# Kernel tuning notes

Hardware: AMD Instinct MI355X
Metric: run time of the kernel (lower is better)

## Reference

```python
import jax, jax.numpy as jnp
from jax import lax
import numpy as np

T, B, HIDDEN, MLPW, DATA = 256, 4096, 64, 128, 8
TSCALE = 1.0

def lipswish(x):
    return 0.909 * jax.nn.silu(x)

def setup_inputs() -> dict:
    key = jax.random.key(0)
    ks = jax.random.split(key, 8)
    def lin(k, i, o):
        return jax.random.normal(k, (i, o), jnp.float32) / np.float32(np.sqrt(i))
    inp = dict(
        ts=jnp.linspace(0.0, 1.0, T, dtype=jnp.float32),
        batch_size=B,
        dW=jax.random.normal(ks[0], (T - 1, B, HIDDEN), jnp.float32),
        drift_W0=lin(ks[1], 1 + HIDDEN, MLPW), drift_b0=jnp.zeros((MLPW,), jnp.float32),
        drift_W1=lin(ks[2], MLPW, MLPW),       drift_b1=jnp.zeros((MLPW,), jnp.float32),
        drift_Wo=lin(ks[3], MLPW, HIDDEN),     drift_bo=jnp.zeros((HIDDEN,), jnp.float32),
        diff_W0=lin(ks[4], 1 + HIDDEN, MLPW),  diff_b0=jnp.zeros((MLPW,), jnp.float32),
        diff_W1=lin(ks[5], MLPW, MLPW),        diff_b1=jnp.zeros((MLPW,), jnp.float32),
        diff_Wo=lin(ks[6], MLPW, HIDDEN),      diff_bo=jnp.zeros((HIDDEN,), jnp.float32),
        readout_W=lin(ks[7], HIDDEN, DATA),    readout_b=jnp.zeros((DATA,), jnp.float32),
    )
    return inp

def reference(ts, batch_size, dW,
              drift_W0, drift_b0, drift_W1, drift_b1, drift_Wo, drift_bo,
              diff_W0, diff_b0, diff_W1, diff_b1, diff_Wo, diff_bo,
              readout_W, readout_b):
    dt = ts[1] - ts[0]  # uniform grid, dt_scale = 1.0

    def mlp(tx, W0, b0, W1, b1, Wo, bo):
        h = lipswish(tx @ W0 + b0)
        h = lipswish(h @ W1 + b1)
        return TSCALE * jnp.tanh(h @ Wo + bo)  # tanh-clamped output

    def f_and_g(t, x):
        tcol = t * jnp.ones((x.shape[0], 1), x.dtype)
        tx = jnp.concatenate([tcol, x], axis=1)  # (B, 1+H)
        f = mlp(tx, drift_W0, drift_b0, drift_W1, drift_b1, drift_Wo, drift_bo)
        g = mlp(tx, diff_W0, diff_b0, diff_W1, diff_b1, diff_Wo, diff_bo)  # diagonal noise
        return f, g

    x0 = jnp.ones((batch_size, HIDDEN), jnp.float32)  # fixed initial point
    f0, g0 = f_and_g(ts[0], x0)
    dWs = dW * jnp.sqrt(dt)  # Brownian increments N(0, dt)

    # Reversible Heun (Stratonovich):
    #   zhat_{n+1} = 2 z_n - zhat_n + f(t_n, zhat_n) dt + g(t_n, zhat_n) dW_n
    #   z_{n+1}    = z_n + 0.5 (f_n + f_{n+1}) dt + 0.5 (g_n + g_{n+1}) dW_n
    def step(carry, inp):
        z, zhat, f, g = carry
        t_next, dw = inp
        zhat_n = 2.0 * z - zhat + f * dt + g * dw
        f_n, g_n = f_and_g(t_next, zhat_n)
        z_n = z + 0.5 * (f + f_n) * dt + 0.5 * (g + g_n) * dw
        return (z_n, zhat_n, f_n, g_n), z_n

    _, zs = lax.scan(step, (x0, x0, f0, g0), (ts[1:], dWs))
    xs = jnp.concatenate([x0[None], zs], axis=0)  # (T, B, H)
    ys = jnp.einsum('tbh,hd->tbd', xs, readout_W) + readout_b  # (T, B, D)
    ys = ys.transpose(1, 0, 2)  # (B, T, D)
    ts_e = jnp.broadcast_to(ts[None, :, None], (batch_size, ts.shape[0], 1))
    # linear_interpolation_coeffs on NaN-free data returns the values unchanged
    return jnp.concatenate([ts_e, ys], axis=2)  # (B, T, 1+D)
```

## Files before the change

### kernel.cpp

```cpp
#include <hip/hip_runtime.h>
#include <math.h>

#define T_STEPS 256
#define BATCH   4096
#define HID     64
#define MW      128
#define DOUT    8
#define RPB     16
#define NTH     512
#define AS      72
#define HS      136

typedef _Float16 half8 __attribute__((ext_vector_type(8)));
typedef float    f32x4 __attribute__((ext_vector_type(4)));

__device__ __forceinline__ float fast_rcp(float x) { return __builtin_amdgcn_rcpf(x); }
__device__ __forceinline__ float lipswish(float x) {
    float e = __expf(-x);
    return 0.909f * x * fast_rcp(1.0f + e);
}
__device__ __forceinline__ float fast_tanh(float x) {
    float e = __expf(2.0f * x);
    return 1.0f - 2.0f * fast_rcp(e + 1.0f);
}

#define MFMA(a, b, c) __builtin_amdgcn_mfma_f32_16x16x32_f16((a), (b), (c), 0, 0, 0)


__global__ __launch_bounds__(NTH, 1)
void sde_kernel(const float* __restrict__ ts,
                const float* __restrict__ dW,
                const float* __restrict__ dW0, const float* __restrict__ db0,
                const float* __restrict__ dW1, const float* __restrict__ db1,
                const float* __restrict__ dWo, const float* __restrict__ dbo,
                const float* __restrict__ gW0, const float* __restrict__ gb0,
                const float* __restrict__ gW1, const float* __restrict__ gb1,
                const float* __restrict__ gWo, const float* __restrict__ gbo,
                const float* __restrict__ rW,  const float* __restrict__ rb,
                float* __restrict__ out)
{
    __shared__ _Float16 Ain_hi[RPB][AS];
    __shared__ _Float16 Ain_lo[RPB][AS];
    __shared__ _Float16 h1b[2][RPB][HS];
    __shared__ _Float16 h2b[2][RPB][HS];
    __shared__ _Float16 zb[2][RPB][AS];
    __shared__ float    bias1t[2 * MW];
    __shared__ float    tsS[T_STEPS];

    const int tid  = threadIdx.x;
    const int lane = tid & 63;
    const int wid  = tid >> 6;
    const int l15  = lane & 15;
    const int quad = lane >> 4;
    const int mlp  = wid >> 2;
    const int nq   = wid & 3;
    const int rowbase = blockIdx.x * RPB;

    for (int i = tid; i < T_STEPS; i += NTH) tsS[i] = ts[i];

    const float t0   = ts[0];
    const float dt   = ts[1] - t0;
    const float sqdt = sqrtf(dt);

    const float* W0 = mlp ? gW0 : dW0;
    const float* W1 = mlp ? gW1 : dW1;

    half8 bw1[2][2], bw2[4][2];
    #pragma unroll
    for (int kt = 0; kt < 2; ++kt)
        #pragma unroll
        for (int nt = 0; nt < 2; ++nt) {
            half8 v;
            #pragma unroll
            for (int j = 0; j < 8; ++j) {
                const int k = kt * 32 + quad * 8 + j;
                const int n = nq * 32 + nt * 16 + l15;
                v[j] = (_Float16)W0[(1 + k) * MW + n];
            }
            bw1[kt][nt] = v;
        }
    #pragma unroll
    for (int kt = 0; kt < 4; ++kt)
        #pragma unroll
        for (int nt = 0; nt < 2; ++nt) {
            half8 v;
            #pragma unroll
            for (int j = 0; j < 8; ++j) {
                const int k = kt * 32 + quad * 8 + j;
                const int n = nq * 32 + nt * 16 + l15;
                v[j] = (_Float16)W1[k * MW + n];
            }
            bw2[kt][nt] = v;
        }

    float b2v[2];
    {
        const float* b1p = mlp ? gb1 : db1;
        #pragma unroll
        for (int nt = 0; nt < 2; ++nt) b2v[nt] = b1p[nq * 32 + nt * 16 + l15];
    }

    const int ucol = nq * 16 + l15;
    const int urow = quad * 4;

    half8 bw3f[4], bw3g[4];
    float b3f = 0.0f, b3g = 0.0f;
    float z[4], zh[4], fold[4], gold[4], dwr[4], dn[4];
    if (wid < 4) {
        #pragma unroll
        for (int kt = 0; kt < 4; ++kt) {
            half8 vf, vg;
            #pragma unroll
            for (int j = 0; j < 8; ++j) {
                const int k = kt * 32 + quad * 8 + j;
                vf[j] = (_Float16)dWo[k * HID + ucol];
                vg[j] = (_Float16)gWo[k * HID + ucol];
            }
            bw3f[kt] = vf;
            bw3g[kt] = vg;
        }
        b3f = dbo[ucol];
        b3g = gbo[ucol];
        #pragma unroll
        for (int i = 0; i < 4; ++i) {
            z[i] = 1.0f; zh[i] = 1.0f; dwr[i] = 0.0f;
            dn[i] = dW[(size_t)(rowbase + urow + i) * HID + ucol];
            Ain_hi[urow + i][ucol] = (_Float16)1.0f;
            Ain_lo[urow + i][ucol] = (_Float16)0.0f;
        }
    }

    half8 brd[2];
    float rbv = 0.0f;
    int   ocol = 0;
    if (wid == 4) {
        #pragma unroll
        for (int kt = 0; kt < 2; ++kt) {
            half8 v;
            #pragma unroll
            for (int j = 0; j < 8; ++j) {
                const int k = kt * 32 + quad * 8 + j;
                v[j] = (l15 < 8) ? (_Float16)rW[k * DOUT + l15] : (_Float16)0.0f;
            }
            brd[kt] = v;
        }
        rbv  = (l15 < 8) ? rb[l15] : 0.0f;
        ocol = (l15 == 8) ? 0 : (l15 + 1);
    }

    float b0s = 0.0f, w0s = 0.0f;
    if (tid >= 256) {
        const int idx = tid - 256;
        b0s = (idx < MW ? db0 : gb0)[idx & (MW - 1)];
        w0s = (idx < MW ? dW0 : gW0)[idx & (MW - 1)];
        bias1t[idx] = b0s + t0 * w0s;
    }
    __syncthreads();

    for (int n = 1; n <= T_STEPS; ++n) {
        {
            const int koff = quad * 8;
            half8 ah[2], al[2];
            #pragma unroll
            for (int kt = 0; kt < 2; ++kt) {
                ah[kt] = *(const half8*)&Ain_hi[l15][kt * 32 + koff];
                al[kt] = *(const half8*)&Ain_lo[l15][kt * 32 + koff];
            }
            f32x4 acc[2];
            #pragma unroll
            for (int nt = 0; nt < 2; ++nt) {
                const float b = bias1t[mlp * MW + nq * 32 + nt * 16 + l15];
                acc[nt] = (f32x4){b, b, b, b};
            }
            #pragma unroll
            for (int nt = 0; nt < 2; ++nt)
                #pragma unroll
                for (int kt = 0; kt < 2; ++kt) {
                    acc[nt] = MFMA(ah[kt], bw1[kt][nt], acc[nt]);
                    acc[nt] = MFMA(al[kt], bw1[kt][nt], acc[nt]);
                }
            #pragma unroll
            for (int nt = 0; nt < 2; ++nt)
                #pragma unroll
                for (int i2 = 0; i2 < 4; ++i2) {
                    const float v = lipswish(acc[nt][i2]);
                    h1b[mlp][quad * 4 + i2][nq * 32 + nt * 16 + l15] = (_Float16)v;
                }
        }
        __syncthreads();

        {
            half8 a[4];
            #pragma unroll
            for (int kt = 0; kt < 4; ++kt)
                a[kt] = *(const half8*)&h1b[mlp][l15][kt * 32 + quad * 8];
            f32x4 acc[2];
            #pragma unroll
            for (int nt = 0; nt < 2; ++nt)
                acc[nt] = (f32x4){b2v[nt], b2v[nt], b2v[nt], b2v[nt]};
            #pragma unroll
            for (int nt = 0; nt < 2; ++nt)
                #pragma unroll
                for (int kt = 0; kt < 4; ++kt)
                    acc[nt] = MFMA(a[kt], bw2[kt][nt], acc[nt]);
            #pragma unroll
            for (int nt = 0; nt < 2; ++nt)
                #pragma unroll
                for (int i2 = 0; i2 < 4; ++i2) {
                    const float v = lipswish(acc[nt][i2]);
                    h2b[mlp][quad * 4 + i2][nq * 32 + nt * 16 + l15] = (_Float16)v;
                }
        }
        __syncthreads();

        if (wid < 4) {
            half8 a[4];
            #pragma unroll
            for (int kt = 0; kt < 4; ++kt)
                a[kt] = *(const half8*)&h2b[0][l15][kt * 32 + quad * 8];
            f32x4 accF = (f32x4){b3f, b3f, b3f, b3f};
            #pragma unroll
            for (int kt = 0; kt < 4; ++kt)
                accF = MFMA(a[kt], bw3f[kt], accF);
            #pragma unroll
            for (int kt = 0; kt < 4; ++kt)
                a[kt] = *(const half8*)&h2b[1][l15][kt * 32 + quad * 8];
            f32x4 accG = (f32x4){b3g, b3g, b3g, b3g};
            #pragma unroll
            for (int kt = 0; kt < 4; ++kt)
                accG = MFMA(a[kt], bw3g[kt], accG);

            const int p = n & 1;
            const int np = (n < T_STEPS - 2) ? n : (T_STEPS - 2);
            #pragma unroll
            for (int i = 0; i < 4; ++i) {
                const float fn = fast_tanh(accF[i]);
                const float gn = fast_tanh(accG[i]);
                if (n > 1)
                    z[i] += 0.5f * (fold[i] + fn) * dt + 0.5f * (gold[i] + gn) * dwr[i];
                zb[p][urow + i][ucol] = (_Float16)z[i];
                if (n < T_STEPS) {
                    dwr[i] = dn[i] * sqdt;
                    dn[i]  = dW[(size_t)np * (BATCH * HID)
                                + (size_t)(rowbase + urow + i) * HID + ucol];
                    zh[i]  = 2.0f * z[i] - zh[i] + fn * dt + gn * dwr[i];
                    const _Float16 hi = (_Float16)zh[i];
                    Ain_hi[urow + i][ucol] = hi;
                    Ain_lo[urow + i][ucol] = (_Float16)(zh[i] - (float)hi);
                }
                fold[i] = fn; gold[i] = gn;
            }
        } else {
            if (wid == 4 && n >= 2) {
                const int koff = quad * 8, q = (n - 1) & 1, s = n - 2;
                half8 a0 = *(const half8*)&zb[q][l15][koff];
                half8 a1 = *(const half8*)&zb[q][l15][32 + koff];
                f32x4 racc = (f32x4){rbv, rbv, rbv, rbv};
                racc = MFMA(a0, brd[0], racc);
                racc = MFMA(a1, brd[1], racc);
                if (l15 < 9) {
                    const float tv = tsS[s];
                    #pragma unroll
                    for (int i2 = 0; i2 < 4; ++i2) {
                        const int r = quad * 4 + i2;
                        out[(size_t)(rowbase + r) * (T_STEPS * 9) + s * 9 + ocol]
                            = (l15 < 8) ? racc[i2] : tv;
                    }
                }
            }
            if (n < T_STEPS) bias1t[tid - 256] = b0s + tsS[n] * w0s;
        }
        __syncthreads();
    }

    if (wid == 4) {
        const int koff = quad * 8, s = T_STEPS - 1;
        half8 a0 = *(const half8*)&zb[0][l15][koff];
        half8 a1 = *(const half8*)&zb[0][l15][32 + koff];
        f32x4 racc = (f32x4){rbv, rbv, rbv, rbv};
        racc = MFMA(a0, brd[0], racc);
        racc = MFMA(a1, brd[1], racc);
        if (l15 < 9) {
            const float tv = tsS[s];
            #pragma unroll
            for (int i2 = 0; i2 < 4; ++i2) {
                const int r = quad * 4 + i2;
                out[(size_t)(rowbase + r) * (T_STEPS * 9) + s * 9 + ocol]
                    = (l15 < 8) ? racc[i2] : tv;
            }
        }
    }
}

extern "C" void kernel_launch(void* const* d_in, const int* in_sizes, int n_in,
                              void* d_out, int out_size, void* d_ws, size_t ws_size,
                              hipStream_t stream) {
    const float* ts  = (const float*)d_in[0];
    const float* dW  = (const float*)d_in[2];
    const float* dW0 = (const float*)d_in[3];
    const float* db0 = (const float*)d_in[4];
    const float* dW1 = (const float*)d_in[5];
    const float* db1 = (const float*)d_in[6];
    const float* dWo = (const float*)d_in[7];
    const float* dbo = (const float*)d_in[8];
    const float* gW0 = (const float*)d_in[9];
    const float* gb0 = (const float*)d_in[10];
    const float* gW1 = (const float*)d_in[11];
    const float* gb1 = (const float*)d_in[12];
    const float* gWo = (const float*)d_in[13];
    const float* gbo = (const float*)d_in[14];
    const float* rW  = (const float*)d_in[15];
    const float* rb  = (const float*)d_in[16];
    float* out = (float*)d_out;

    sde_kernel<<<dim3(BATCH / RPB), dim3(NTH), 0, stream>>>(
        ts, dW, dW0, db0, dW1, db1, dWo, dbo,
        gW0, gb0, gW1, gb1, gWo, gbo, rW, rb, out);
}
```

Measured before the change: 681.9 us.

## Transpose MFMA operands so outputs are row-contiguous and fold lipswish scale into weights

```diff
diff --git a/kernel.cpp b/kernel.cpp
--- a/kernel.cpp
+++ b/kernel.cpp
@@ -12,12 +12,13 @@
 #define HS      136
 
 typedef _Float16 half8 __attribute__((ext_vector_type(8)));
+typedef _Float16 half4 __attribute__((ext_vector_type(4)));
 typedef float    f32x4 __attribute__((ext_vector_type(4)));
 
 __device__ __forceinline__ float fast_rcp(float x) { return __builtin_amdgcn_rcpf(x); }
-__device__ __forceinline__ float lipswish(float x) {
+__device__ __forceinline__ float silu(float x) {
     float e = __expf(-x);
-    return 0.909f * x * fast_rcp(1.0f + e);
+    return x * fast_rcp(1.0f + e);
 }
 __device__ __forceinline__ float fast_tanh(float x) {
     float e = __expf(2.0f * x);
@@ -39,13 +40,13 @@
                 const float* __restrict__ rW,  const float* __restrict__ rb,
                 float* __restrict__ out)
 {
-    __shared__ _Float16 Ain_hi[RPB][AS];
-    __shared__ _Float16 Ain_lo[RPB][AS];
-    __shared__ _Float16 h1b[2][RPB][HS];
-    __shared__ _Float16 h2b[2][RPB][HS];
-    __shared__ _Float16 zb[2][RPB][AS];
-    __shared__ float    bias1t[2 * MW];
-    __shared__ float    tsS[T_STEPS];
+    __shared__ __align__(16) _Float16 Ain_hi[RPB][AS];
+    __shared__ __align__(16) _Float16 Ain_lo[RPB][AS];
+    __shared__ __align__(16) _Float16 h1b[2][RPB][HS];
+    __shared__ __align__(16) _Float16 h2b[2][RPB][HS];
+    __shared__ __align__(16) _Float16 zb[2][RPB][AS];
+    __shared__ __align__(16) float    bias1t[2 * MW];
+    __shared__ float tsS[T_STEPS];
 
     const int tid  = threadIdx.x;
     const int lane = tid & 63;
@@ -74,8 +75,8 @@
             #pragma unroll
             for (int j = 0; j < 8; ++j) {
                 const int k = kt * 32 + quad * 8 + j;
-                const int n = nq * 32 + nt * 16 + l15;
-                v[j] = (_Float16)W0[(1 + k) * MW + n];
+                const int m = nq * 32 + nt * 16 + l15;
+                v[j] = (_Float16)W0[(1 + k) * MW + m];
             }
             bw1[kt][nt] = v;
         }
@@ -87,24 +88,24 @@
             #pragma unroll
             for (int j = 0; j < 8; ++j) {
                 const int k = kt * 32 + quad * 8 + j;
-                const int n = nq * 32 + nt * 16 + l15;
-                v[j] = (_Float16)W1[k * MW + n];
+                const int m = nq * 32 + nt * 16 + l15;
+                v[j] = (_Float16)(0.909f * W1[k * MW + m]);
             }
             bw2[kt][nt] = v;
         }
 
-    float b2v[2];
+    f32x4 b2v4[2];
     {
         const float* b1p = mlp ? gb1 : db1;
         #pragma unroll
-        for (int nt = 0; nt < 2; ++nt) b2v[nt] = b1p[nq * 32 + nt * 16 + l15];
-    }
-
-    const int ucol = nq * 16 + l15;
-    const int urow = quad * 4;
+        for (int nt = 0; nt < 2; ++nt)
+            b2v4[nt] = *(const f32x4*)&b1p[nq * 32 + nt * 16 + quad * 4];
+    }
+
+    const int dbase = (wid & 3) * 16 + quad * 4;
 
     half8 bw3f[4], bw3g[4];
-    float b3f = 0.0f, b3g = 0.0f;
+    f32x4 b3f4 = {0,0,0,0}, b3g4 = {0,0,0,0};
     float z[4], zh[4], fold[4], gold[4], dwr[4], dn[4];
     if (wid < 4) {
         #pragma unroll
@@ -113,26 +114,29 @@
             #pragma unroll
             for (int j = 0; j < 8; ++j) {
                 const int k = kt * 32 + quad * 8 + j;
-                vf[j] = (_Float16)dWo[k * HID + ucol];
-                vg[j] = (_Float16)gWo[k * HID + ucol];
+                const int m = wid * 16 + l15;
+                vf[j] = (_Float16)(0.909f * dWo[k * HID + m]);
+                vg[j] = (_Float16)(0.909f * gWo[k * HID + m]);
             }
             bw3f[kt] = vf;
             bw3g[kt] = vg;
         }
-        b3f = dbo[ucol];
-        b3g = gbo[ucol];
+        b3f4 = *(const f32x4*)&dbo[dbase];
+        b3g4 = *(const f32x4*)&gbo[dbase];
+        f32x4 d0 = *(const f32x4*)&dW[(size_t)(rowbase + l15) * HID + dbase];
         #pragma unroll
         for (int i = 0; i < 4; ++i) {
-            z[i] = 1.0f; zh[i] = 1.0f; dwr[i] = 0.0f;
-            dn[i] = dW[(size_t)(rowbase + urow + i) * HID + ucol];
-            Ain_hi[urow + i][ucol] = (_Float16)1.0f;
-            Ain_lo[urow + i][ucol] = (_Float16)0.0f;
-        }
+            z[i] = 1.0f; zh[i] = 1.0f; dwr[i] = 0.0f; dn[i] = d0[i];
+        }
+        half4 ones, zeros;
+        #pragma unroll
+        for (int i = 0; i < 4; ++i) { ones[i] = (_Float16)1.0f; zeros[i] = (_Float16)0.0f; }
+        *(half4*)&Ain_hi[l15][dbase] = ones;
+        *(half4*)&Ain_lo[l15][dbase] = zeros;
     }
 
     half8 brd[2];
-    float rbv = 0.0f;
-    int   ocol = 0;
+    f32x4 rbv4 = {0,0,0,0};
     if (wid == 4) {
         #pragma unroll
         for (int kt = 0; kt < 2; ++kt) {
@@ -144,8 +148,7 @@
             }
             brd[kt] = v;
         }
-        rbv  = (l15 < 8) ? rb[l15] : 0.0f;
-        ocol = (l15 == 8) ? 0 : (l15 + 1);
+        if (quad < 2) rbv4 = *(const f32x4*)&rb[quad * 4];
     }
 
     float b0s = 0.0f, w0s = 0.0f;
@@ -157,115 +160,128 @@
     }
     __syncthreads();
 
+    const int koff = quad * 8;
+
     for (int n = 1; n <= T_STEPS; ++n) {
         {
-            const int koff = quad * 8;
-            half8 ah[2], al[2];
+            half8 bh[2], bl[2];
             #pragma unroll
             for (int kt = 0; kt < 2; ++kt) {
-                ah[kt] = *(const half8*)&Ain_hi[l15][kt * 32 + koff];
-                al[kt] = *(const half8*)&Ain_lo[l15][kt * 32 + koff];
+                bh[kt] = *(const half8*)&Ain_hi[l15][kt * 32 + koff];
+                bl[kt] = *(const half8*)&Ain_lo[l15][kt * 32 + koff];
             }
             f32x4 acc[2];
             #pragma unroll
+            for (int nt = 0; nt < 2; ++nt)
+                acc[nt] = *(const f32x4*)&bias1t[mlp * MW + nq * 32 + nt * 16 + quad * 4];
+            #pragma unroll
+            for (int nt = 0; nt < 2; ++nt)
+                #pragma unroll
+                for (int kt = 0; kt < 2; ++kt) {
+                    acc[nt] = MFMA(bw1[kt][nt], bh[kt], acc[nt]);
+                    acc[nt] = MFMA(bw1[kt][nt], bl[kt], acc[nt]);
+                }
+            #pragma unroll
             for (int nt = 0; nt < 2; ++nt) {
-                const float b = bias1t[mlp * MW + nq * 32 + nt * 16 + l15];
-                acc[nt] = (f32x4){b, b, b, b};
-            }
+                half4 hv;
+                #pragma unroll
+                for (int i2 = 0; i2 < 4; ++i2) hv[i2] = (_Float16)silu(acc[nt][i2]);
+                *(half4*)&h1b[mlp][l15][nq * 32 + nt * 16 + quad * 4] = hv;
+            }
+        }
+        __syncthreads();
+
+        {
+            half8 b_[4];
+            #pragma unroll
+            for (int kt = 0; kt < 4; ++kt)
+                b_[kt] = *(const half8*)&h1b[mlp][l15][kt * 32 + koff];
+            f32x4 acc[2];
+            #pragma unroll
+            for (int nt = 0; nt < 2; ++nt) acc[nt] = b2v4[nt];
             #pragma unroll
             for (int nt = 0; nt < 2; ++nt)
                 #pragma unroll
-                for (int kt = 0; kt < 2; ++kt) {
-                    acc[nt] = MFMA(ah[kt], bw1[kt][nt], acc[nt]);
-                    acc[nt] = MFMA(al[kt], bw1[kt][nt], acc[nt]);
+                for (int kt = 0; kt < 4; ++kt)
+                    acc[nt] = MFMA(bw2[kt][nt], b_[kt], acc[nt]);
+            #pragma unroll
+            for (int nt = 0; nt < 2; ++nt) {
+                half4 hv;
+                #pragma unroll
+                for (int i2 = 0; i2 < 4; ++i2) hv[i2] = (_Float16)silu(acc[nt][i2]);
+                *(half4*)&h2b[mlp][l15][nq * 32 + nt * 16 + quad * 4] = hv;
+            }
+        }
+        __syncthreads();
+
+        if (wid < 4) {
+            half8 b_[4];
+            #pragma unroll
+            for (int kt = 0; kt < 4; ++kt)
+                b_[kt] = *(const half8*)&h2b[0][l15][kt * 32 + koff];
+            f32x4 accF = b3f4;
+            #pragma unroll
+            for (int kt = 0; kt < 4; ++kt)
+                accF = MFMA(bw3f[kt], b_[kt], accF);
+            #pragma unroll
+            for (int kt = 0; kt < 4; ++kt)
+                b_[kt] = *(const half8*)&h2b[1][l15][kt * 32 + koff];
+            f32x4 accG = b3g4;
+            #pragma unroll
+            for (int kt = 0; kt < 4; ++kt)
+                accG = MFMA(bw3g[kt], b_[kt], accG);
+
+            const int p = n & 1;
+            float fn[4], gn[4];
+            #pragma unroll
+            for (int i = 0; i < 4; ++i) {
+                fn[i] = fast_tanh(accF[i]);
+                gn[i] = fast_tanh(accG[i]);
+            }
+            if (n > 1) {
+                #pragma unroll
+                for (int i = 0; i < 4; ++i)
+                    z[i] += 0.5f * (fold[i] + fn[i]) * dt + 0.5f * (gold[i] + gn[i]) * dwr[i];
+            }
+            half4 zp;
+            #pragma unroll
+            for (int i = 0; i < 4; ++i) zp[i] = (_Float16)z[i];
+            *(half4*)&zb[p][l15][dbase] = zp;
+
+            if (n < T_STEPS) {
+                const int np = (n < T_STEPS - 2) ? n : (T_STEPS - 2);
+                f32x4 dn4 = *(const f32x4*)&dW[(size_t)np * (BATCH * HID)
+                                               + (size_t)(rowbase + l15) * HID + dbase];
+                half4 hip, lop;
+                #pragma unroll
+                for (int i = 0; i < 4; ++i) {
+                    dwr[i] = dn[i] * sqdt;
+                    dn[i]  = dn4[i];
+                    zh[i]  = 2.0f * z[i] - zh[i] + fn[i] * dt + gn[i] * dwr[i];
+                    const _Float16 hi = (_Float16)zh[i];
+                    hip[i] = hi;
+                    lop[i] = (_Float16)(zh[i] - (float)hi);
                 }
-            #pragma unroll
-            for (int nt = 0; nt < 2; ++nt)
-                #pragma unroll
-                for (int i2 = 0; i2 < 4; ++i2) {
-                    const float v = lipswish(acc[nt][i2]);
-                    h1b[mlp][quad * 4 + i2][nq * 32 + nt * 16 + l15] = (_Float16)v;
-                }
-        }
-        __syncthreads();
-
-        {
-            half8 a[4];
-            #pragma unroll
-            for (int kt = 0; kt < 4; ++kt)
-                a[kt] = *(const half8*)&h1b[mlp][l15][kt * 32 + quad * 8];
-            f32x4 acc[2];
-            #pragma unroll
-            for (int nt = 0; nt < 2; ++nt)
-                acc[nt] = (f32x4){b2v[nt], b2v[nt], b2v[nt], b2v[nt]};
-            #pragma unroll
-            for (int nt = 0; nt < 2; ++nt)
-                #pragma unroll
-                for (int kt = 0; kt < 4; ++kt)
-                    acc[nt] = MFMA(a[kt], bw2[kt][nt], acc[nt]);
-            #pragma unroll
-            for (int nt = 0; nt < 2; ++nt)
-                #pragma unroll
-                for (int i2 = 0; i2 < 4; ++i2) {
-                    const float v = lipswish(acc[nt][i2]);
-                    h2b[mlp][quad * 4 + i2][nq * 32 + nt * 16 + l15] = (_Float16)v;
-                }
-        }
-        __syncthreads();
-
-        if (wid < 4) {
-            half8 a[4];
-            #pragma unroll
-            for (int kt = 0; kt < 4; ++kt)
-                a[kt] = *(const half8*)&h2b[0][l15][kt * 32 + quad * 8];
-            f32x4 accF = (f32x4){b3f, b3f, b3f, b3f};
-            #pragma unroll
-            for (int kt = 0; kt < 4; ++kt)
-                accF = MFMA(a[kt], bw3f[kt], accF);
-            #pragma unroll
-            for (int kt = 0; kt < 4; ++kt)
-                a[kt] = *(const half8*)&h2b[1][l15][kt * 32 + quad * 8];
-            f32x4 accG = (f32x4){b3g, b3g, b3g, b3g};
-            #pragma unroll
-            for (int kt = 0; kt < 4; ++kt)
-                accG = MFMA(a[kt], bw3g[kt], accG);
-
-            const int p = n & 1;
-            const int np = (n < T_STEPS - 2) ? n : (T_STEPS - 2);
-            #pragma unroll
-            for (int i = 0; i < 4; ++i) {
-                const float fn = fast_tanh(accF[i]);
-                const float gn = fast_tanh(accG[i]);
-                if (n > 1)
-                    z[i] += 0.5f * (fold[i] + fn) * dt + 0.5f * (gold[i] + gn) * dwr[i];
-                zb[p][urow + i][ucol] = (_Float16)z[i];
-                if (n < T_STEPS) {
-                    dwr[i] = dn[i] * sqdt;
-                    dn[i]  = dW[(size_t)np * (BATCH * HID)
-                                + (size_t)(rowbase + urow + i) * HID + ucol];
-                    zh[i]  = 2.0f * z[i] - zh[i] + fn * dt + gn * dwr[i];
-                    const _Float16 hi = (_Float16)zh[i];
-                    Ain_hi[urow + i][ucol] = hi;
-                    Ain_lo[urow + i][ucol] = (_Float16)(zh[i] - (float)hi);
-                }
-                fold[i] = fn; gold[i] = gn;
-            }
+                *(half4*)&Ain_hi[l15][dbase] = hip;
+                *(half4*)&Ain_lo[l15][dbase] = lop;
+            }
+            #pragma unroll
+            for (int i = 0; i < 4; ++i) { fold[i] = fn[i]; gold[i] = gn[i]; }
         } else {
             if (wid == 4 && n >= 2) {
-                const int koff = quad * 8, q = (n - 1) & 1, s = n - 2;
-                half8 a0 = *(const half8*)&zb[q][l15][koff];
-                half8 a1 = *(const half8*)&zb[q][l15][32 + koff];
-                f32x4 racc = (f32x4){rbv, rbv, rbv, rbv};
-                racc = MFMA(a0, brd[0], racc);
-                racc = MFMA(a1, brd[1], racc);
-                if (l15 < 9) {
-                    const float tv = tsS[s];
+                const int q = (n - 1) & 1, s = n - 2;
+                half8 z0 = *(const half8*)&zb[q][l15][koff];
+                half8 z1 = *(const half8*)&zb[q][l15][32 + koff];
+                f32x4 racc = rbv4;
+                racc = MFMA(brd[0], z0, racc);
+                racc = MFMA(brd[1], z1, racc);
+                float* orow = out + (size_t)(rowbase + l15) * (T_STEPS * 9) + (size_t)s * 9;
+                if (quad < 2) {
                     #pragma unroll
-                    for (int i2 = 0; i2 < 4; ++i2) {
-                        const int r = quad * 4 + i2;
-                        out[(size_t)(rowbase + r) * (T_STEPS * 9) + s * 9 + ocol]
-                            = (l15 < 8) ? racc[i2] : tv;
-                    }
+                    for (int i2 = 0; i2 < 4; ++i2)
+                        orow[1 + quad * 4 + i2] = racc[i2];
+                } else if (quad == 2) {
+                    orow[0] = tsS[s];
                 }
             }
             if (n < T_STEPS) bias1t[tid - 256] = b0s + tsS[n] * w0s;
@@ -274,20 +290,19 @@
     }
 
     if (wid == 4) {
-        const int koff = quad * 8, s = T_STEPS - 1;
-        half8 a0 = *(const half8*)&zb[0][l15][koff];
-        half8 a1 = *(const half8*)&zb[0][l15][32 + koff];
-        f32x4 racc = (f32x4){rbv, rbv, rbv, rbv};
-        racc = MFMA(a0, brd[0], racc);
-        racc = MFMA(a1, brd[1], racc);
-        if (l15 < 9) {
-            const float tv = tsS[s];
-            #pragma unroll
-            for (int i2 = 0; i2 < 4; ++i2) {
-                const int r = quad * 4 + i2;
-                out[(size_t)(rowbase + r) * (T_STEPS * 9) + s * 9 + ocol]
-                    = (l15 < 8) ? racc[i2] : tv;
-            }
+        const int s = T_STEPS - 1;
+        half8 z0 = *(const half8*)&zb[0][l15][koff];
+        half8 z1 = *(const half8*)&zb[0][l15][32 + koff];
+        f32x4 racc = rbv4;
+        racc = MFMA(brd[0], z0, racc);
+        racc = MFMA(brd[1], z1, racc);
+        float* orow = out + (size_t)(rowbase + l15) * (T_STEPS * 9) + (size_t)s * 9;
+        if (quad < 2) {
+            #pragma unroll
+            for (int i2 = 0; i2 < 4; ++i2)
+                orow[1 + quad * 4 + i2] = racc[i2];
+        } else if (quad == 2) {
+            orow[0] = tsS[s];
         }
     }
 }
```

After: 747.8 us. 1.1x slower.

## Double block threads so each wave computes one 16-column MLP tile; fold lipswish scale into weights

Applied to the files above, without the earlier changes.

```diff
diff --git a/kernel.cpp b/kernel.cpp
--- a/kernel.cpp
+++ b/kernel.cpp
@@ -7,7 +7,7 @@
 #define MW      128
 #define DOUT    8
 #define RPB     16
-#define NTH     512
+#define NTH     1024
 #define AS      72
 #define HS      136
 
@@ -15,9 +15,9 @@
 typedef float    f32x4 __attribute__((ext_vector_type(4)));
 
 __device__ __forceinline__ float fast_rcp(float x) { return __builtin_amdgcn_rcpf(x); }
-__device__ __forceinline__ float lipswish(float x) {
+__device__ __forceinline__ float silu(float x) {
     float e = __expf(-x);
-    return 0.909f * x * fast_rcp(1.0f + e);
+    return x * fast_rcp(1.0f + e);
 }
 __device__ __forceinline__ float fast_tanh(float x) {
     float e = __expf(2.0f * x);
@@ -52,8 +52,9 @@
     const int wid  = tid >> 6;
     const int l15  = lane & 15;
     const int quad = lane >> 4;
-    const int mlp  = wid >> 2;
-    const int nq   = wid & 3;
+    const int mlp  = wid >> 3;
+    const int oct  = wid & 7;
+    const int cb   = oct * 16;
     const int rowbase = blockIdx.x * RPB;
 
     for (int i = tid; i < T_STEPS; i += NTH) tsS[i] = ts[i];
@@ -65,42 +66,31 @@
     const float* W0 = mlp ? gW0 : dW0;
     const float* W1 = mlp ? gW1 : dW1;
 
-    half8 bw1[2][2], bw2[4][2];
+    half8 bw1[2], bw2[4];
     #pragma unroll
-    for (int kt = 0; kt < 2; ++kt)
-        #pragma unroll
-        for (int nt = 0; nt < 2; ++nt) {
-            half8 v;
-            #pragma unroll
-            for (int j = 0; j < 8; ++j) {
-                const int k = kt * 32 + quad * 8 + j;
-                const int n = nq * 32 + nt * 16 + l15;
-                v[j] = (_Float16)W0[(1 + k) * MW + n];
-            }
-            bw1[kt][nt] = v;
-        }
+    for (int kt = 0; kt < 2; ++kt) {
+        half8 v;
+        #pragma unroll
+        for (int j = 0; j < 8; ++j) {
+            const int k = kt * 32 + quad * 8 + j;
+            v[j] = (_Float16)W0[(1 + k) * MW + cb + l15];
+        }
+        bw1[kt] = v;
+    }
     #pragma unroll
-    for (int kt = 0; kt < 4; ++kt)
-        #pragma unroll
-        for (int nt = 0; nt < 2; ++nt) {
-            half8 v;
-            #pragma unroll
-            for (int j = 0; j < 8; ++j) {
-                const int k = kt * 32 + quad * 8 + j;
-                const int n = nq * 32 + nt * 16 + l15;
-                v[j] = (_Float16)W1[k * MW + n];
-            }
-            bw2[kt][nt] = v;
-        }
-
-    float b2v[2];
-    {
-        const float* b1p = mlp ? gb1 : db1;
-        #pragma unroll
-        for (int nt = 0; nt < 2; ++nt) b2v[nt] = b1p[nq * 32 + nt * 16 + l15];
-    }
-
-    const int ucol = nq * 16 + l15;
+    for (int kt = 0; kt < 4; ++kt) {
+        half8 v;
+        #pragma unroll
+        for (int j = 0; j < 8; ++j) {
+            const int k = kt * 32 + quad * 8 + j;
+            v[j] = (_Float16)(0.909f * W1[k * MW + cb + l15]);
+        }
+        bw2[kt] = v;
+    }
+
+    const float b2v = (mlp ? gb1 : db1)[cb + l15];
+
+    const int ucol = (wid & 3) * 16 + l15;
     const int urow = quad * 4;
 
     half8 bw3f[4], bw3g[4];
@@ -113,8 +103,8 @@
             #pragma unroll
             for (int j = 0; j < 8; ++j) {
                 const int k = kt * 32 + quad * 8 + j;
-                vf[j] = (_Float16)dWo[k * HID + ucol];
-                vg[j] = (_Float16)gWo[k * HID + ucol];
+                vf[j] = (_Float16)(0.909f * dWo[k * HID + ucol]);
+                vg[j] = (_Float16)(0.909f * gWo[k * HID + ucol]);
             }
             bw3f[kt] = vf;
             bw3g[kt] = vg;
@@ -149,43 +139,34 @@
     }
 
     float b0s = 0.0f, w0s = 0.0f;
-    if (tid >= 256) {
-        const int idx = tid - 256;
+    if (tid >= 768) {
+        const int idx = tid - 768;
         b0s = (idx < MW ? db0 : gb0)[idx & (MW - 1)];
         w0s = (idx < MW ? dW0 : gW0)[idx & (MW - 1)];
         bias1t[idx] = b0s + t0 * w0s;
     }
     __syncthreads();
 
+    const int koff = quad * 8;
+
     for (int n = 1; n <= T_STEPS; ++n) {
         {
-            const int koff = quad * 8;
             half8 ah[2], al[2];
             #pragma unroll
             for (int kt = 0; kt < 2; ++kt) {
                 ah[kt] = *(const half8*)&Ain_hi[l15][kt * 32 + koff];
                 al[kt] = *(const half8*)&Ain_lo[l15][kt * 32 + koff];
             }
-            f32x4 acc[2];
-            #pragma unroll
-            for (int nt = 0; nt < 2; ++nt) {
-                const float b = bias1t[mlp * MW + nq * 32 + nt * 16 + l15];
-                acc[nt] = (f32x4){b, b, b, b};
-            }
-            #pragma unroll
-            for (int nt = 0; nt < 2; ++nt)
-                #pragma unroll
-                for (int kt = 0; kt < 2; ++kt) {
-                    acc[nt] = MFMA(ah[kt], bw1[kt][nt], acc[nt]);
-                    acc[nt] = MFMA(al[kt], bw1[kt][nt], acc[nt]);
-                }
-            #pragma unroll
-            for (int nt = 0; nt < 2; ++nt)
-                #pragma unroll
-                for (int i2 = 0; i2 < 4; ++i2) {
-                    const float v = lipswish(acc[nt][i2]);
-                    h1b[mlp][quad * 4 + i2][nq * 32 + nt * 16 + l15] = (_Float16)v;
-                }
+            const float b = bias1t[mlp * MW + cb + l15];
+            f32x4 acc = (f32x4){b, b, b, b};
+            #pragma unroll
+            for (int kt = 0; kt < 2; ++kt) {
+                acc = MFMA(ah[kt], bw1[kt], acc);
+                acc = MFMA(al[kt], bw1[kt], acc);
+            }
+            #pragma unroll
+            for (int i2 = 0; i2 < 4; ++i2)
+                h1b[mlp][quad * 4 + i2][cb + l15] = (_Float16)silu(acc[i2]);
         }
         __syncthreads();
 
@@ -193,23 +174,14 @@
             half8 a[4];
             #pragma unroll
             for (int kt = 0; kt < 4; ++kt)
-                a[kt] = *(const half8*)&h1b[mlp][l15][kt * 32 + quad * 8];
-            f32x4 acc[2];
-            #pragma unroll
-            for (int nt = 0; nt < 2; ++nt)
-                acc[nt] = (f32x4){b2v[nt], b2v[nt], b2v[nt], b2v[nt]};
-            #pragma unroll
-            for (int nt = 0; nt < 2; ++nt)
-                #pragma unroll
-                for (int kt = 0; kt < 4; ++kt)
-                    acc[nt] = MFMA(a[kt], bw2[kt][nt], acc[nt]);
-            #pragma unroll
-            for (int nt = 0; nt < 2; ++nt)
-                #pragma unroll
-                for (int i2 = 0; i2 < 4; ++i2) {
-                    const float v = lipswish(acc[nt][i2]);
-                    h2b[mlp][quad * 4 + i2][nq * 32 + nt * 16 + l15] = (_Float16)v;
-                }
+                a[kt] = *(const half8*)&h1b[mlp][l15][kt * 32 + koff];
+            f32x4 acc = (f32x4){b2v, b2v, b2v, b2v};
+            #pragma unroll
+            for (int kt = 0; kt < 4; ++kt)
+                acc = MFMA(a[kt], bw2[kt], acc);
+            #pragma unroll
+            for (int i2 = 0; i2 < 4; ++i2)
+                h2b[mlp][quad * 4 + i2][cb + l15] = (_Float16)silu(acc[i2]);
         }
         __syncthreads();
 
@@ -217,14 +189,14 @@
             half8 a[4];
             #pragma unroll
             for (int kt = 0; kt < 4; ++kt)
-                a[kt] = *(const half8*)&h2b[0][l15][kt * 32 + quad * 8];
+                a[kt] = *(const half8*)&h2b[0][l15][kt * 32 + koff];
             f32x4 accF = (f32x4){b3f, b3f, b3f, b3f};
             #pragma unroll
             for (int kt = 0; kt < 4; ++kt)
                 accF = MFMA(a[kt], bw3f[kt], accF);
             #pragma unroll
             for (int kt = 0; kt < 4; ++kt)
-                a[kt] = *(const half8*)&h2b[1][l15][kt * 32 + quad * 8];
+                a[kt] = *(const half8*)&h2b[1][l15][kt * 32 + koff];
             f32x4 accG = (f32x4){b3g, b3g, b3g, b3g};
             #pragma unroll
             for (int kt = 0; kt < 4; ++kt)
@@ -250,9 +222,9 @@
                 }
                 fold[i] = fn; gold[i] = gn;
             }
-        } else {
-            if (wid == 4 && n >= 2) {
-                const int koff = quad * 8, q = (n - 1) & 1, s = n - 2;
+        } else if (wid == 4) {
+            if (n >= 2) {
+                const int q = (n - 1) & 1, s = n - 2;
                 half8 a0 = *(const half8*)&zb[q][l15][koff];
                 half8 a1 = *(const half8*)&zb[q][l15][32 + koff];
                 f32x4 racc = (f32x4){rbv, rbv, rbv, rbv};
@@ -268,13 +240,14 @@
                     }
                 }
             }
-            if (n < T_STEPS) bias1t[tid - 256] = b0s + tsS[n] * w0s;
+        } else if (wid >= 12) {
+            if (n < T_STEPS) bias1t[tid - 768] = b0s + tsS[n] * w0s;
         }
         __syncthreads();
     }
 
     if (wid == 4) {
-        const int koff = quad * 8, s = T_STEPS - 1;
+        const int s = T_STEPS - 1;
         half8 a0 = *(const half8*)&zb[0][l15][koff];
         half8 a1 = *(const half8*)&zb[0][l15][32 + koff];
         f32x4 racc = (f32x4){rbv, rbv, rbv, rbv};
```

Result: slower. 867.7 us (+27.3%).
